# Performance work log

Measured on AMD Instinct MI355X. Metric: run time of the kernel, lower is better.

The kernel has to match this reference:

```python
import jax, jax.numpy as jnp
import numpy as np

B, C, N, H = 8, 256, 2048, 4
DIM = C // H
EPS = 1e-5
SLOPE = 0.2


def conv1x1(W, b, x):
    # W: [out, in], x: [B, in, N] -> [B, out, N]
    return jnp.einsum('oc,bcn->bon', W, x) + b[None, :, None]


def setup_inputs() -> dict:
    key = jax.random.key(0)
    ks = jax.random.split(key, 16)
    s = 1.0 / np.sqrt(C)
    s2 = 1.0 / np.sqrt(2 * C)
    return {
        'init_query': jax.random.normal(ks[0], (B, C, N), jnp.float32),
        'key': jax.random.normal(ks[1], (B, C, N), jnp.float32),
        'value': jax.random.normal(ks[2], (B, C, N), jnp.float32),
        'Wq': jax.random.normal(ks[3], (C, C), jnp.float32) * s,
        'bq': jax.random.normal(ks[4], (C,), jnp.float32) * s,
        'Wk': jax.random.normal(ks[5], (C, C), jnp.float32) * s,
        'bk': jax.random.normal(ks[6], (C,), jnp.float32) * s,
        'Wv': jax.random.normal(ks[7], (C, C), jnp.float32) * s,
        'bv': jax.random.normal(ks[8], (C,), jnp.float32) * s,
        'Wm': jax.random.normal(ks[9], (C, C), jnp.float32) * s,
        'bm': jax.random.normal(ks[10], (C,), jnp.float32) * s,
        'W1': jax.random.normal(ks[11], (2 * C, 2 * C), jnp.float32) * s2,
        'b1': jax.random.normal(ks[12], (2 * C,), jnp.float32) * s2,
        'gamma': jnp.ones((2 * C,), jnp.float32),
        'beta': jnp.zeros((2 * C,), jnp.float32),
        'W2': jax.random.normal(ks[13], (C, 2 * C), jnp.float32) * s2,
        'b2': jnp.zeros((C,), jnp.float32),  # nn.init.constant_(bias, 0.0)
    }


def reference(init_query, key, value, Wq, bq, Wk, bk, Wv, bv, Wm, bm, W1, b1, gamma, beta, W2, b2):
    # projections, then view [B, C, N] -> [B, dim, H, N] (dim outermost, matching torch .view)
    q = conv1x1(Wq, bq, init_query).reshape(B, DIM, H, N)
    k = conv1x1(Wk, bk, key).reshape(B, DIM, H, N)
    v = conv1x1(Wv, bv, value).reshape(B, DIM, H, N)
    scores = jnp.einsum('bdhn,bdhm->bhnm', q, k) / jnp.sqrt(jnp.float32(DIM))
    attn = jax.nn.softmax(scores, axis=-1)  # [B, H, N, N]
    x = jnp.einsum('bhnm,bdhm->bdhn', attn, v).reshape(B, C, N)
    x = conv1x1(Wm, bm, x)
    # post_merge: conv1x1 -> BatchNorm1d (training-mode batch stats) -> LeakyReLU(0.2) -> conv1x1
    h = conv1x1(W1, b1, jnp.concatenate([x, init_query], axis=1))  # [B, 2C, N]
    mu = jnp.mean(h, axis=(0, 2), keepdims=True)
    var = jnp.mean(jnp.square(h - mu), axis=(0, 2), keepdims=True)  # biased var, as torch BN
    hn = (h - mu) / jnp.sqrt(var + EPS) * gamma[None, :, None] + beta[None, :, None]
    hn = jnp.where(hn > 0, hn, SLOPE * hn)
    out = conv1x1(W2, b2, hn)
    return (out, attn)
```

## Files before the change

### kernel.cpp

```cpp
#include <hip/hip_runtime.h>
#include <stdint.h>

typedef __bf16 bf16x8 __attribute__((ext_vector_type(8)));
typedef float f32x4 __attribute__((ext_vector_type(4)));

constexpr int NB = 8;
constexpr int NC = 256;
constexpr int NN = 2048;
constexpr int NH = 4;
constexpr int ND = 64;
constexpr int NC2 = 512;
constexpr size_t TND = (size_t)NB * NN * NC;
__device__ constexpr float C2 = 0.125f * 1.4426950408889634f;

__device__ __forceinline__ ushort f2bf(float f) {
  union { float f; uint32_t u; } x; x.f = f;
  return (ushort)((x.u + 0x7FFFu + ((x.u >> 16) & 1u)) >> 16);
}
__device__ __forceinline__ float bf2f(ushort h) {
  union { uint32_t u; float f; } x; x.u = (uint32_t)h << 16;
  return x.f;
}

__device__ __forceinline__ void bar_lds() {
  __builtin_amdgcn_sched_barrier(0);
  asm volatile("s_waitcnt lgkmcnt(0)" ::: "memory");
  __builtin_amdgcn_s_barrier();
  __builtin_amdgcn_sched_barrier(0);
}


__global__ void k_cast_all(const float* __restrict__ Wq, const float* __restrict__ Wk,
                           const float* __restrict__ Wv, const float* __restrict__ Wm,
                           const float* __restrict__ W1, const float* __restrict__ W2,
                           ushort* __restrict__ wqkv, ushort* __restrict__ wm_b,
                           ushort* __restrict__ w1_b, ushort* __restrict__ w2_b) {
  int i = blockIdx.x * 256 + threadIdx.x;
  if (i < 196608) {
    int op = i >> 16, j = i & 65535;
    int r = j >> 8, c = j & 255;
    const float* s = op == 0 ? Wq : op == 1 ? Wk : Wv;
    int orig = op < 2 ? (((r & 63) << 2) | (r >> 6)) : r;
    wqkv[i] = f2bf(s[orig * NC + c]);
  } else if (i < 262144) {
    int j = i - 196608;
    int co = j >> 8, jj = j & 255;
    wm_b[j] = f2bf(Wm[co * NC + (jj & 63) * NH + (jj >> 6)]);
  } else if (i < 524288) {
    int j = i - 262144;
    w1_b[j] = f2bf(W1[j]);
  } else {
    int j = i - 524288;
    w2_b[j] = f2bf(W2[j]);
  }
}

__global__ void k_bn_finalize(const float* __restrict__ stats, const float* __restrict__ gamma,
                              const float* __restrict__ beta, float4* __restrict__ aff) {
  int c = blockIdx.x * 256 + threadIdx.x;
  if (c >= NC2) return;
  const float inv_n = 1.f / (float)(NB * NN);
  float mu  = stats[c * 2] * inv_n;
  float var = stats[c * 2 + 1] * inv_n - mu * mu;
  float isg = gamma[c] * rsqrtf(var + 1e-5f);
  aff[c] = make_float4(mu, isg, beta[c], 0.f);
}


__device__ __forceinline__ bf16x8 ldtile(const ushort* base, int lr, int lg, int fc, int ks) {
  int row = fc * 16 + lr;
  int u = (ks * 4 + lg) ^ (lr & 7);
  return *(const bf16x8*)((const char*)base + row * 128 + u * 16);
}

__global__ __launch_bounds__(512, 4) void k_attn(
    const ushort* __restrict__ qt, const ushort* __restrict__ kt,
    const ushort* __restrict__ vnat, float* __restrict__ attn,
    ushort* __restrict__ xT) {
  __shared__ ushort Kl[2][4096];
  __shared__ ushort Vl[2][4096];
  __shared__ ushort Pl[8192];

  const int tid = threadIdx.x;
  const int lane = tid & 63, w = tid >> 6;
  const int lr = lane & 15, lg = lane >> 4;

  int flat = blockIdx.x;
  int xcd = flat & 7, idx = flat >> 3;
  int z = xcd * 4 + (idx >> 4);
  int r0 = (idx & 15) * 128;
  int b = z >> 2, h = z & 3;

  const ushort* kbase = kt + (size_t)z * NN * ND;
  const ushort* vbase = vnat + ((size_t)b * NC + h) * NN;

  const int sr0 = tid >> 3, sc0 = tid & 7;
  const int d0 = sr0 * 128 + ((sc0 ^ (sr0 & 7)) << 4);

  bf16x8 aq0, aq1;
  {
    const ushort* qp = qt + ((size_t)z * NN + r0 + w * 16 + lr) * ND;
    aq0 = *(const bf16x8*)(qp + lg * 8);
    aq1 = *(const bf16x8*)(qp + 32 + lg * 8);
  }

  uint4 gk0, gv0;

  gk0 = *(const uint4*)(kbase + (size_t)sr0 * ND + sc0 * 8);
  *(uint4*)((char*)Kl[0] + d0) = gk0;
  gk0 = *(const uint4*)(kbase + (size_t)(64 + sr0) * ND + sc0 * 8);
  bar_lds();

  float m_ln[4], s_ln[4];
#pragma unroll
  for (int j = 0; j < 4; ++j) { m_ln[j] = -INFINITY; s_ln[j] = 0.f; }

  for (int t = 0; t < 32; ++t) {
    int kb = t & 1;
    if (t < 31) *(uint4*)((char*)Kl[kb ^ 1] + d0) = gk0;
    if (t < 30)
      gk0 = *(const uint4*)(kbase + ((size_t)(t + 2) * 64 + sr0) * ND + sc0 * 8);
    f32x4 sa[4] = {};
#pragma unroll
    for (int ks = 0; ks < 2; ++ks) {
      bf16x8 aqk = ks ? aq1 : aq0;
#pragma unroll
      for (int fc = 0; fc < 4; ++fc)
        sa[fc] = __builtin_amdgcn_mfma_f32_16x16x32_bf16(aqk, ldtile(Kl[kb], lr, lg, fc, ks), sa[fc], 0, 0, 0);
    }
#pragma unroll
    for (int j = 0; j < 4; ++j) {
      float tm = fmaxf(fmaxf(sa[0][j], sa[1][j]), fmaxf(sa[2][j], sa[3][j]));
      float mn = fmaxf(m_ln[j], tm);
      float mnC = mn * C2;
      float es = exp2f(fmaf(sa[0][j], C2, -mnC)) + exp2f(fmaf(sa[1][j], C2, -mnC))
               + exp2f(fmaf(sa[2][j], C2, -mnC)) + exp2f(fmaf(sa[3][j], C2, -mnC));
      s_ln[j] = s_ln[j] * exp2f(fmaf(m_ln[j], C2, -mnC)) + es;
      m_ln[j] = mn;
    }
    bar_lds();
  }

  float mC[4];
#pragma unroll
  for (int j = 0; j < 4; ++j) {
    float m = m_ln[j];
#pragma unroll
    for (int o = 1; o < 16; o <<= 1) m = fmaxf(m, __shfl_xor(m, o));
    float c = s_ln[j] * exp2f((m_ln[j] - m) * C2);
#pragma unroll
    for (int o = 1; o < 16; o <<= 1) c += __shfl_xor(c, o);
    mC[j] = m * C2 + __log2f(c);
  }

  gk0 = *(const uint4*)(kbase + (size_t)sr0 * ND + sc0 * 8);
  gv0 = *(const uint4*)(vbase + (size_t)sr0 * 4 * NN + sc0 * 8);
  *(uint4*)((char*)Kl[0] + d0) = gk0;
  *(uint4*)((char*)Vl[0] + d0) = gv0;
  gk0 = *(const uint4*)(kbase + (size_t)(64 + sr0) * ND + sc0 * 8);
  gv0 = *(const uint4*)(vbase + (size_t)sr0 * 4 * NN + 64 + sc0 * 8);
  bar_lds();

  f32x4 acc[4] = {};
  const int prow = w * 16 + lr;
  char* plb = (char*)Pl;
  for (int t = 0; t < 32; ++t) {
    int kb = t & 1;
    if (t < 31) {
      *(uint4*)((char*)Kl[kb ^ 1] + d0) = gk0;
      *(uint4*)((char*)Vl[kb ^ 1] + d0) = gv0;
    }
    if (t < 30) {
      gk0 = *(const uint4*)(kbase + ((size_t)(t + 2) * 64 + sr0) * ND + sc0 * 8);
      gv0 = *(const uint4*)(vbase + (size_t)sr0 * 4 * NN + (t + 2) * 64 + sc0 * 8);
    }
    f32x4 sa[4] = {};
#pragma unroll
    for (int ks = 0; ks < 2; ++ks) {
      bf16x8 aqk = ks ? aq1 : aq0;
#pragma unroll
      for (int fc = 0; fc < 4; ++fc)
        sa[fc] = __builtin_amdgcn_mfma_f32_16x16x32_bf16(aqk, ldtile(Kl[kb], lr, lg, fc, ks), sa[fc], 0, 0, 0);
    }
#pragma unroll
    for (int fc = 0; fc < 4; ++fc)
#pragma unroll
      for (int j = 0; j < 4; ++j) {
        int row = w * 16 + lg * 4 + j;
        float p = exp2f(fmaf(sa[fc][j], C2, -mC[j]));
        int byte = (row << 7) + ((fc * 16 + lr) << 1);
        byte ^= (row & 7) << 4;
        *(ushort*)(plb + byte) = f2bf(p);
      }
    float* abase = attn + ((size_t)z * NN + r0) * NN + t * 64;
#pragma unroll
    for (int k = 0; k < 4; ++k) {
      int row = w * 16 + lg + k * 4;
      int byte = (row << 7) + (lr << 3);
      byte ^= (row & 7) << 4;
      const ushort* pq = (const ushort*)(plb + byte);
      f32x4 vv = { bf2f(pq[0]), bf2f(pq[1]), bf2f(pq[2]), bf2f(pq[3]) };
      __builtin_nontemporal_store(vv, (f32x4*)(abase + (size_t)row * NN + lr * 4));
    }
#pragma unroll
    for (int ks = 0; ks < 2; ++ks) {
      int abyte = (prow << 7) + ks * 64 + lg * 16;
      abyte ^= (prow & 7) << 4;
      bf16x8 ap = *(const bf16x8*)(plb + abyte);
#pragma unroll
      for (int fc = 0; fc < 4; ++fc)
        acc[fc] = __builtin_amdgcn_mfma_f32_16x16x32_bf16(ap, ldtile(Vl[kb], lr, lg, fc, ks), acc[fc], 0, 0, 0);
    }
    bar_lds();
  }
#pragma unroll
  for (int fc = 0; fc < 4; ++fc)
#pragma unroll
    for (int j = 0; j < 4; ++j) {
      int n = r0 + w * 16 + lg * 4 + j;
      xT[((size_t)b * NN + n) * NC + h * 64 + fc * 16 + lr] = f2bf(acc[fc][j]);
    }
}


enum GemmMode { M_PROJ = 0, M_WM, M_W1, M_W2 };

template <int MODE>
__global__ __launch_bounds__(256) void k_gemm(
    const ushort* __restrict__ A, const ushort* __restrict__ Bm,
    const float* __restrict__ Fa, const float* __restrict__ Fb, const float* __restrict__ Fc,
    const float* __restrict__ b0, const float* __restrict__ b1v, const float* __restrict__ b2v,
    const float4* __restrict__ aff, float* __restrict__ stats,
    float* __restrict__ outf, ushort* __restrict__ outb, ushort* __restrict__ outb2) {
  constexpr int BR = (MODE == M_WM || MODE == M_W1) ? 64 : 128;
  constexpr int BC = (MODE == M_W1) ? 256 : (MODE == M_W2) ? 64 : 128;
  constexpr int KT = (MODE == M_PROJ || MODE == M_WM) ? 256 : 512;
  constexpr int FR = BR / 32;
  constexpr int FC = BC / 32;
  constexpr int LDL = 72;

  __shared__ ushort ldsU[BR * LDL + BC * LDL];
  ushort* ldsA = ldsU;
  ushort* ldsB = ldsU + BR * LDL;

  const int tid = threadIdx.x;
  const int lane = tid & 63, wave = tid >> 6;
  const int wr = (wave >> 1) * (FR * 16), wc = (wave & 1) * (FC * 16);
  const int lr = lane & 15, lg = lane >> 4, lk = lg * 8;
  const int c0 = blockIdx.x * BC, r0 = blockIdx.y * BR;
  const int op = (MODE == M_PROJ) ? (int)(blockIdx.z >> 3) : 0;
  const size_t z = (MODE == M_PROJ) ? (blockIdx.z & 7) : blockIdx.z;

  auto stage_t = [&](ushort* dst, const float* src, int ROWS) {
    int n = tid & (ROWS - 1), cgb = tid / ROWS;
    int gpp = 256 / ROWS;
    for (int u = 0; u < 8 / gpp; ++u) {
      int cg = cgb + u * gpp;
      union { ushort us[8]; uint4 v; } pk;
#pragma unroll
      for (int e = 0; e < 8; ++e)
        pk.us[e] = f2bf(src[(size_t)(cg * 8 + e) * NN + n]);
      *(uint4*)&dst[n * LDL + cg * 8] = pk.v;
    }
  };

  f32x4 acc[FR][FC] = {};

  for (int kk = 0; kk < KT; kk += 64) {
    if constexpr (MODE == M_W1) {
      if (kk < NC) {
        const ushort* src = A + (z * NN + r0) * (size_t)NC + kk;
#pragma unroll
        for (int i = 0; i < BR / 32; ++i) {
          int off = (tid + i * 256) * 8, row = off >> 6, k = off & 63;
          *(uint4*)&ldsA[row * LDL + k] = *(const uint4*)(src + (size_t)row * NC + k);
        }
      } else {
        stage_t(ldsA, Fa + ((size_t)z * NC + (kk - NC)) * NN + r0, BR);
      }
    } else {
      const ushort* src; int ld;
      if constexpr (MODE == M_PROJ)        { src = A + (size_t)op * NC * NC + (size_t)r0 * NC + kk; ld = NC; }
      else if constexpr (MODE == M_WM)     { src = A + (z * NN + r0) * (size_t)NC + kk; ld = NC; }
      else                                  { src = A + (size_t)r0 * NC2 + kk; ld = NC2; }
#pragma unroll
      for (int i = 0; i < BR / 32; ++i) {
        int off = (tid + i * 256) * 8, row = off >> 6, k = off & 63;
        *(uint4*)&ldsA[row * LDL + k] = *(const uint4*)(src + (size_t)row * ld + k);
      }
    }
    if constexpr (MODE == M_PROJ) {
      const float* Fsel = op == 0 ? Fa : op == 1 ? Fb : Fc;
      stage_t(ldsB, Fsel + ((size_t)z * NC + kk) * NN + c0, BC);
    } else if constexpr (MODE == M_W2) {
      const ushort* src = Bm + (z * NN + c0) * (size_t)NC2 + kk;
#pragma unroll
      for (int i = 0; i < BC / 32; ++i) {
        int off = (tid + i * 256) * 8, row = off >> 6, k = off & 63;
        union { ushort u[8]; uint4 v; } t, o;
        t.v = *(const uint4*)(src + (size_t)row * NC2 + k);
#pragma unroll
        for (int e = 0; e < 8; ++e) {
          float4 pr = aff[kk + k + e];
          float y = (bf2f(t.u[e]) - pr.x) * pr.y + pr.z;
          y = y > 0.f ? y : 0.2f * y;
          o.u[e] = f2bf(y);
        }
        *(uint4*)&ldsB[row * LDL + k] = o.v;
      }
    } else {
      const ushort* src; int ld;
      if constexpr (MODE == M_WM)          { src = Bm + (size_t)c0 * NC + kk; ld = NC; }
      else                                  { src = Bm + (size_t)c0 * NC2 + kk; ld = NC2; }
#pragma unroll
      for (int i = 0; i < BC / 32; ++i) {
        int off = (tid + i * 256) * 8, row = off >> 6, k = off & 63;
        *(uint4*)&ldsB[row * LDL + k] = *(const uint4*)(src + (size_t)row * ld + k);
      }
    }
    __syncthreads();
#pragma unroll
    for (int ks = 0; ks < 2; ++ks) {
      bf16x8 afr[FR], bfr[FC];
#pragma unroll
      for (int fr = 0; fr < FR; ++fr)
        afr[fr] = *(const bf16x8*)&ldsA[(wr + fr * 16 + lr) * LDL + ks * 32 + lk];
#pragma unroll
      for (int fc = 0; fc < FC; ++fc)
        bfr[fc] = *(const bf16x8*)&ldsB[(wc + fc * 16 + lr) * LDL + ks * 32 + lk];
#pragma unroll
      for (int fr = 0; fr < FR; ++fr)
#pragma unroll
        for (int fc = 0; fc < FC; ++fc)
          acc[fr][fc] = __builtin_amdgcn_mfma_f32_16x16x32_bf16(afr[fr], bfr[fc], acc[fr][fc], 0, 0, 0);
    }
    __syncthreads();
  }

  if constexpr (MODE == M_PROJ) {
    if (op < 2) {
      const float* bb = op == 0 ? b0 : b1v;
      char* tb = (char*)ldsU;
#pragma unroll
      for (int fr = 0; fr < FR; ++fr)
#pragma unroll
        for (int fc = 0; fc < FC; ++fc) {
          int n_l = wc + fc * 16 + lr;
          int rb = wr + fr * 16 + lg * 4;
          union { ushort u[4]; uint2 v; } pk;
#pragma unroll
          for (int j = 0; j < 4; ++j) {
            int r = r0 + rb + j;
            pk.u[j] = f2bf(acc[fr][fc][j] + bb[((r & 63) << 2) | (r >> 6)]);
          }
          int byte = n_l * 256 + rb * 2;
          byte ^= (n_l & 7) << 4;
          *(uint2*)(tb + byte) = pk.v;
        }
      __syncthreads();
      ushort* dst = outb + (size_t)op * TND;
#pragma unroll
      for (int hh = 0; hh < 2; ++hh) {
        size_t zz = z * 4 + (r0 >> 6) + hh;
#pragma unroll
        for (int u = 0; u < 4; ++u) {
          int seg = u * 256 + tid;
          int n_l = seg >> 3, dd = (seg & 7) * 8;
          int byte = n_l * 256 + (hh * 64 + dd) * 2;
          byte ^= (n_l & 7) << 4;
          uint4 v = *(const uint4*)(tb + byte);
          *(uint4*)(dst + (zz * NN + c0 + n_l) * (size_t)ND + dd) = v;
        }
      }
    } else {
#pragma unroll
      for (int fr = 0; fr < FR; ++fr)
#pragma unroll
        for (int fc = 0; fc < FC; ++fc)
#pragma unroll
          for (int j = 0; j < 4; ++j) {
            int r = r0 + wr + fr * 16 + lg * 4 + j;
            int c = c0 + wc + fc * 16 + lr;
            outb2[(z * NC + r) * (size_t)NN + c] = f2bf(acc[fr][fc][j] + b2v[r]);
          }
    }
    return;
  }

  float sfc[FC], qfc[FC];
#pragma unroll
  for (int fc = 0; fc < FC; ++fc) { sfc[fc] = 0.f; qfc[fc] = 0.f; }
#pragma unroll
  for (int fr = 0; fr < FR; ++fr)
#pragma unroll
    for (int fc = 0; fc < FC; ++fc)
#pragma unroll
      for (int j = 0; j < 4; ++j) {
        int r = r0 + wr + fr * 16 + lg * 4 + j;
        int c = c0 + wc + fc * 16 + lr;
        float v = acc[fr][fc][j];
        if constexpr (MODE == M_WM) {
          v += b0[c];
          outb[(z * NN + r) * (size_t)NC + c] = f2bf(v);
        } else if constexpr (MODE == M_W1) {
          v += b0[c];
          outb[(z * NN + r) * (size_t)NC2 + c] = f2bf(v);
          sfc[fc] += v; qfc[fc] += v * v;
        } else {
          v += b0[r];
          outf[(z * NC + r) * (size_t)NN + c] = v;
        }
      }
  if constexpr (MODE == M_W1) {
#pragma unroll
    for (int fc = 0; fc < FC; ++fc) {
      float s1 = sfc[fc], s2 = qfc[fc];
      s1 += __shfl_xor(s1, 16); s1 += __shfl_xor(s1, 32);
      s2 += __shfl_xor(s2, 16); s2 += __shfl_xor(s2, 32);
      if (lane < 16) {
        int ch = c0 + wc + fc * 16 + lane;
        atomicAdd(&stats[ch * 2],     s1);
        atomicAdd(&stats[ch * 2 + 1], s2);
      }
    }
  }
}


extern "C" void kernel_launch(void* const* d_in, const int* in_sizes, int n_in,
                              void* d_out, int out_size, void* d_ws, size_t ws_size,
                              hipStream_t stream) {
  const float* iq    = (const float*)d_in[0];
  const float* keyi  = (const float*)d_in[1];
  const float* vali  = (const float*)d_in[2];
  const float* Wq = (const float*)d_in[3];  const float* bq = (const float*)d_in[4];
  const float* Wk = (const float*)d_in[5];  const float* bk = (const float*)d_in[6];
  const float* Wv = (const float*)d_in[7];  const float* bv = (const float*)d_in[8];
  const float* Wm = (const float*)d_in[9];  const float* bm = (const float*)d_in[10];
  const float* W1 = (const float*)d_in[11]; const float* b1 = (const float*)d_in[12];
  const float* gamma = (const float*)d_in[13]; const float* beta = (const float*)d_in[14];
  const float* W2 = (const float*)d_in[15]; const float* b2 = (const float*)d_in[16];

  float* out  = (float*)d_out;
  float* attn = out + (size_t)NB * NC * NN;

  uint8_t* cur = (uint8_t*)d_ws;
  auto alloc = [&](size_t bytes) { uint8_t* p = cur; cur += (bytes + 255) & ~(size_t)255; return p; };
  ushort* wqkv  = (ushort*)alloc((size_t)NC * NC * 2 * 3);
  ushort* wm_b  = (ushort*)alloc((size_t)NC * NC * 2);
  ushort* w1_b  = (ushort*)alloc((size_t)NC2 * NC2 * 2);
  ushort* w2_b  = (ushort*)alloc((size_t)NC * NC2 * 2);
  ushort* qtkt  = (ushort*)alloc(TND * 2 * 2);
  ushort* v_nat = (ushort*)alloc(TND * 2);
  ushort* xT    = (ushort*)alloc(TND * 2);
  ushort* xmT   = (ushort*)alloc(TND * 2);
  ushort* hT    = (ushort*)alloc((size_t)NB * NN * NC2 * 2);
  float*  stats = (float*)alloc(NC2 * 2 * 4);
  float4* aff   = (float4*)alloc(NC2 * 16);
  ushort* kt    = qtkt + TND;

  (void)hipMemsetAsync(stats, 0, NC2 * 2 * 4, stream);

  k_cast_all<<<dim3(2560), 256, 0, stream>>>(Wq, Wk, Wv, Wm, W1, W2, wqkv, wm_b, w1_b, w2_b);

  k_gemm<M_PROJ><<<dim3(16, 2, 24), 256, 0, stream>>>(
      wqkv, nullptr, iq, keyi, vali, bq, bk, bv, nullptr, nullptr, nullptr, qtkt, v_nat);

  k_attn<<<dim3(512), 512, 0, stream>>>(qtkt, kt, v_nat, attn, xT);

  k_gemm<M_WM><<<dim3(2, 32, 8), 256, 0, stream>>>(
      xT, wm_b, nullptr, nullptr, nullptr, bm, nullptr, nullptr, nullptr, nullptr, nullptr, xmT, nullptr);

  k_gemm<M_W1><<<dim3(2, 32, 8), 256, 0, stream>>>(
      xmT, w1_b, iq, nullptr, nullptr, b1, nullptr, nullptr, nullptr, stats, nullptr, hT, nullptr);

  k_bn_finalize<<<dim3(2), 256, 0, stream>>>(stats, gamma, beta, aff);

  k_gemm<M_W2><<<dim3(32, 2, 8), 256, 0, stream>>>(
      w2_b, hT, nullptr, nullptr, nullptr, b2, nullptr, nullptr, aff, nullptr, out, nullptr, nullptr);
}
```

Measured before the change: 258.1 us.

## Fuse weight casting and BN finalize into GEMM staging, drop two kernels

Removes the separate weight-cast kernel and the batch-norm finalize kernel. Each GEMM now reads fp32 weights directly and converts them to bf16 while staging into LDS, including the head permutation for the QKV and merge weights. The W2 GEMM computes the BN affine parameters into shared memory in its prologue. This saves two launches and the round trip of the bf16 weight buffers, at the cost of redundant conversion in every block and strided scalar fp32 loads for the Wm permutation.

```diff
diff --git a/kernel.cpp b/kernel.cpp
--- a/kernel.cpp
+++ b/kernel.cpp
@@ -30,43 +30,6 @@
 }
 
 
-__global__ void k_cast_all(const float* __restrict__ Wq, const float* __restrict__ Wk,
-                           const float* __restrict__ Wv, const float* __restrict__ Wm,
-                           const float* __restrict__ W1, const float* __restrict__ W2,
-                           ushort* __restrict__ wqkv, ushort* __restrict__ wm_b,
-                           ushort* __restrict__ w1_b, ushort* __restrict__ w2_b) {
-  int i = blockIdx.x * 256 + threadIdx.x;
-  if (i < 196608) {
-    int op = i >> 16, j = i & 65535;
-    int r = j >> 8, c = j & 255;
-    const float* s = op == 0 ? Wq : op == 1 ? Wk : Wv;
-    int orig = op < 2 ? (((r & 63) << 2) | (r >> 6)) : r;
-    wqkv[i] = f2bf(s[orig * NC + c]);
-  } else if (i < 262144) {
-    int j = i - 196608;
-    int co = j >> 8, jj = j & 255;
-    wm_b[j] = f2bf(Wm[co * NC + (jj & 63) * NH + (jj >> 6)]);
-  } else if (i < 524288) {
-    int j = i - 262144;
-    w1_b[j] = f2bf(W1[j]);
-  } else {
-    int j = i - 524288;
-    w2_b[j] = f2bf(W2[j]);
-  }
-}
-
-__global__ void k_bn_finalize(const float* __restrict__ stats, const float* __restrict__ gamma,
-                              const float* __restrict__ beta, float4* __restrict__ aff) {
-  int c = blockIdx.x * 256 + threadIdx.x;
-  if (c >= NC2) return;
-  const float inv_n = 1.f / (float)(NB * NN);
-  float mu  = stats[c * 2] * inv_n;
-  float var = stats[c * 2 + 1] * inv_n - mu * mu;
-  float isg = gamma[c] * rsqrtf(var + 1e-5f);
-  aff[c] = make_float4(mu, isg, beta[c], 0.f);
-}
-
-
 __device__ __forceinline__ bf16x8 ldtile(const ushort* base, int lr, int lg, int fc, int ks) {
   int row = fc * 16 + lr;
   int u = (ks * 4 + lg) ^ (lr & 7);
@@ -227,10 +190,11 @@
 
 template <int MODE>
 __global__ __launch_bounds__(256) void k_gemm(
-    const ushort* __restrict__ A, const ushort* __restrict__ Bm,
+    const float* __restrict__ W0, const float* __restrict__ W1p, const float* __restrict__ W2p,
+    const ushort* __restrict__ Abf, const ushort* __restrict__ Bbf,
     const float* __restrict__ Fa, const float* __restrict__ Fb, const float* __restrict__ Fc,
     const float* __restrict__ b0, const float* __restrict__ b1v, const float* __restrict__ b2v,
-    const float4* __restrict__ aff, float* __restrict__ stats,
+    float* __restrict__ stats, const float* __restrict__ gamma, const float* __restrict__ beta,
     float* __restrict__ outf, ushort* __restrict__ outb, ushort* __restrict__ outb2) {
   constexpr int BR = (MODE == M_WM || MODE == M_W1) ? 64 : 128;
   constexpr int BC = (MODE == M_W1) ? 256 : (MODE == M_W2) ? 64 : 128;
@@ -240,6 +204,7 @@
   constexpr int LDL = 72;
 
   __shared__ ushort ldsU[BR * LDL + BC * LDL];
+  __shared__ float4 affl[(MODE == M_W2) ? NC2 : 1];
   ushort* ldsA = ldsU;
   ushort* ldsB = ldsU + BR * LDL;
 
@@ -251,6 +216,17 @@
   const int op = (MODE == M_PROJ) ? (int)(blockIdx.z >> 3) : 0;
   const size_t z = (MODE == M_PROJ) ? (blockIdx.z & 7) : blockIdx.z;
 
+  if constexpr (MODE == M_W2) {
+    const float inv_n = 1.f / (float)(NB * NN);
+    for (int c = tid; c < NC2; c += 256) {
+      float mu  = stats[c * 2] * inv_n;
+      float var = stats[c * 2 + 1] * inv_n - mu * mu;
+      float isg = gamma[c] * rsqrtf(var + 1e-5f);
+      affl[c] = make_float4(mu, isg, beta[c], 0.f);
+    }
+    __syncthreads();
+  }
+
   auto stage_t = [&](ushort* dst, const float* src, int ROWS) {
     int n = tid & (ROWS - 1), cgb = tid / ROWS;
     int gpp = 256 / ROWS;
@@ -263,13 +239,38 @@
       *(uint4*)&dst[n * LDL + cg * 8] = pk.v;
     }
   };
+  auto stage_w = [&](ushort* dst, const float* src, int ld, int iters) {
+    for (int i = 0; i < iters; ++i) {
+      int off = (tid + i * 256) * 8, row = off >> 6, k = off & 63;
+      const float* p = src + (size_t)row * ld + k;
+      float4 x0 = *(const float4*)p, x1 = *(const float4*)(p + 4);
+      union { ushort us[8]; uint4 v; } pk;
+      pk.us[0] = f2bf(x0.x); pk.us[1] = f2bf(x0.y); pk.us[2] = f2bf(x0.z); pk.us[3] = f2bf(x0.w);
+      pk.us[4] = f2bf(x1.x); pk.us[5] = f2bf(x1.y); pk.us[6] = f2bf(x1.z); pk.us[7] = f2bf(x1.w);
+      *(uint4*)&dst[row * LDL + k] = pk.v;
+    }
+  };
 
   f32x4 acc[FR][FC] = {};
 
   for (int kk = 0; kk < KT; kk += 64) {
-    if constexpr (MODE == M_W1) {
+    if constexpr (MODE == M_PROJ) {
+      const float* Wsel = op == 0 ? W0 : op == 1 ? W1p : W2p;
+#pragma unroll
+      for (int i = 0; i < BR / 32; ++i) {
+        int off = (tid + i * 256) * 8, row = off >> 6, k = off & 63;
+        int r = r0 + row;
+        int orig = op < 2 ? (((r & 63) << 2) | (r >> 6)) : r;
+        const float* p = Wsel + (size_t)orig * NC + kk + k;
+        float4 x0 = *(const float4*)p, x1 = *(const float4*)(p + 4);
+        union { ushort us[8]; uint4 v; } pk;
+        pk.us[0] = f2bf(x0.x); pk.us[1] = f2bf(x0.y); pk.us[2] = f2bf(x0.z); pk.us[3] = f2bf(x0.w);
+        pk.us[4] = f2bf(x1.x); pk.us[5] = f2bf(x1.y); pk.us[6] = f2bf(x1.z); pk.us[7] = f2bf(x1.w);
+        *(uint4*)&ldsA[row * LDL + k] = pk.v;
+      }
+    } else if constexpr (MODE == M_W1) {
       if (kk < NC) {
-        const ushort* src = A + (z * NN + r0) * (size_t)NC + kk;
+        const ushort* src = Abf + (z * NN + r0) * (size_t)NC + kk;
 #pragma unroll
         for (int i = 0; i < BR / 32; ++i) {
           int off = (tid + i * 256) * 8, row = off >> 6, k = off & 63;
@@ -278,22 +279,34 @@
       } else {
         stage_t(ldsA, Fa + ((size_t)z * NC + (kk - NC)) * NN + r0, BR);
       }
-    } else {
-      const ushort* src; int ld;
-      if constexpr (MODE == M_PROJ)        { src = A + (size_t)op * NC * NC + (size_t)r0 * NC + kk; ld = NC; }
-      else if constexpr (MODE == M_WM)     { src = A + (z * NN + r0) * (size_t)NC + kk; ld = NC; }
-      else                                  { src = A + (size_t)r0 * NC2 + kk; ld = NC2; }
+    } else if constexpr (MODE == M_WM) {
+      const ushort* src = Abf + (z * NN + r0) * (size_t)NC + kk;
 #pragma unroll
       for (int i = 0; i < BR / 32; ++i) {
         int off = (tid + i * 256) * 8, row = off >> 6, k = off & 63;
-        *(uint4*)&ldsA[row * LDL + k] = *(const uint4*)(src + (size_t)row * ld + k);
-      }
+        *(uint4*)&ldsA[row * LDL + k] = *(const uint4*)(src + (size_t)row * NC + k);
+      }
+    } else {
+      stage_w(ldsA, W0 + (size_t)r0 * NC2 + kk, NC2, BR / 32);
     }
     if constexpr (MODE == M_PROJ) {
       const float* Fsel = op == 0 ? Fa : op == 1 ? Fb : Fc;
       stage_t(ldsB, Fsel + ((size_t)z * NC + kk) * NN + c0, BC);
-    } else if constexpr (MODE == M_W2) {
-      const ushort* src = Bm + (z * NN + c0) * (size_t)NC2 + kk;
+    } else if constexpr (MODE == M_WM) {
+      int h0 = kk >> 6;
+#pragma unroll
+      for (int i = 0; i < BC / 32; ++i) {
+        int off = (tid + i * 256) * 8, row = off >> 6, k = off & 63;
+        const float* p = W0 + (size_t)(c0 + row) * NC + h0;
+        union { ushort us[8]; uint4 v; } pk;
+#pragma unroll
+        for (int e = 0; e < 8; ++e) pk.us[e] = f2bf(p[(k + e) * 4]);
+        *(uint4*)&ldsB[row * LDL + k] = pk.v;
+      }
+    } else if constexpr (MODE == M_W1) {
+      stage_w(ldsB, W1p + (size_t)c0 * NC2 + kk, NC2, BC / 32);
+    } else {
+      const ushort* src = Bbf + (z * NN + c0) * (size_t)NC2 + kk;
 #pragma unroll
       for (int i = 0; i < BC / 32; ++i) {
         int off = (tid + i * 256) * 8, row = off >> 6, k = off & 63;
@@ -301,21 +314,12 @@
         t.v = *(const uint4*)(src + (size_t)row * NC2 + k);
 #pragma unroll
         for (int e = 0; e < 8; ++e) {
-          float4 pr = aff[kk + k + e];
+          float4 pr = affl[kk + k + e];
           float y = (bf2f(t.u[e]) - pr.x) * pr.y + pr.z;
           y = y > 0.f ? y : 0.2f * y;
           o.u[e] = f2bf(y);
         }
         *(uint4*)&ldsB[row * LDL + k] = o.v;
-      }
-    } else {
-      const ushort* src; int ld;
-      if constexpr (MODE == M_WM)          { src = Bm + (size_t)c0 * NC + kk; ld = NC; }
-      else                                  { src = Bm + (size_t)c0 * NC2 + kk; ld = NC2; }
-#pragma unroll
-      for (int i = 0; i < BC / 32; ++i) {
-        int off = (tid + i * 256) * 8, row = off >> 6, k = off & 63;
-        *(uint4*)&ldsB[row * LDL + k] = *(const uint4*)(src + (size_t)row * ld + k);
       }
     }
     __syncthreads();
@@ -446,36 +450,31 @@
 
   uint8_t* cur = (uint8_t*)d_ws;
   auto alloc = [&](size_t bytes) { uint8_t* p = cur; cur += (bytes + 255) & ~(size_t)255; return p; };
-  ushort* wqkv  = (ushort*)alloc((size_t)NC * NC * 2 * 3);
-  ushort* wm_b  = (ushort*)alloc((size_t)NC * NC * 2);
-  ushort* w1_b  = (ushort*)alloc((size_t)NC2 * NC2 * 2);
-  ushort* w2_b  = (ushort*)alloc((size_t)NC * NC2 * 2);
   ushort* qtkt  = (ushort*)alloc(TND * 2 * 2);
   ushort* v_nat = (ushort*)alloc(TND * 2);
   ushort* xT    = (ushort*)alloc(TND * 2);
   ushort* xmT   = (ushort*)alloc(TND * 2);
   ushort* hT    = (ushort*)alloc((size_t)NB * NN * NC2 * 2);
   float*  stats = (float*)alloc(NC2 * 2 * 4);
-  float4* aff   = (float4*)alloc(NC2 * 16);
   ushort* kt    = qtkt + TND;
 
   (void)hipMemsetAsync(stats, 0, NC2 * 2 * 4, stream);
 
-  k_cast_all<<<dim3(2560), 256, 0, stream>>>(Wq, Wk, Wv, Wm, W1, W2, wqkv, wm_b, w1_b, w2_b);
-
   k_gemm<M_PROJ><<<dim3(16, 2, 24), 256, 0, stream>>>(
-      wqkv, nullptr, iq, keyi, vali, bq, bk, bv, nullptr, nullptr, nullptr, qtkt, v_nat);
+      Wq, Wk, Wv, nullptr, nullptr, iq, keyi, vali, bq, bk, bv,
+      nullptr, nullptr, nullptr, nullptr, qtkt, v_nat);
 
   k_attn<<<dim3(512), 512, 0, stream>>>(qtkt, kt, v_nat, attn, xT);
 
   k_gemm<M_WM><<<dim3(2, 32, 8), 256, 0, stream>>>(
-      xT, wm_b, nullptr, nullptr, nullptr, bm, nullptr, nullptr, nullptr, nullptr, nullptr, xmT, nullptr);
+      Wm, nullptr, nullptr, xT, nullptr, nullptr, nullptr, nullptr, bm, nullptr, nullptr,
+      nullptr, nullptr, nullptr, nullptr, xmT, nullptr);
 
   k_gemm<M_W1><<<dim3(2, 32, 8), 256, 0, stream>>>(
-      xmT, w1_b, iq, nullptr, nullptr, b1, nullptr, nullptr, nullptr, stats, nullptr, hT, nullptr);
-
-  k_bn_finalize<<<dim3(2), 256, 0, stream>>>(stats, gamma, beta, aff);
+      nullptr, W1, nullptr, xmT, nullptr, iq, nullptr, nullptr, b1, nullptr, nullptr,
+      stats, nullptr, nullptr, nullptr, hT, nullptr);
 
   k_gemm<M_W2><<<dim3(32, 2, 8), 256, 0, stream>>>(
-      w2_b, hT, nullptr, nullptr, nullptr, b2, nullptr, nullptr, aff, nullptr, out, nullptr, nullptr);
-}
+      W2, nullptr, nullptr, nullptr, hT, nullptr, nullptr, nullptr, b2, nullptr, nullptr,
+      stats, gamma, beta, out, nullptr, nullptr);
+}
```

Result: slower. 308.8 us (+19.6%).
